# Optimization experiments

Measured on AMD Instinct MI355X. Metric: run time of the kernel, lower is better.

## Reference

```python
import jax, jax.numpy as jnp
import numpy as np

NUM_HEADS = 6

def setup_inputs() -> dict:
    key = jax.random.key(0)
    k1, k2, k3, k4 = jax.random.split(key, 4)
    B, N, C = 8, 2048, 384
    x = jax.random.normal(k1, (B, N, C), dtype=jnp.float32)
    qkv_w = jax.random.normal(k2, (3 * C, C), dtype=jnp.float32) * (C ** -0.5)
    proj_w = jax.random.normal(k3, (C, C), dtype=jnp.float32) * (C ** -0.5)
    proj_b = jax.random.normal(k4, (C,), dtype=jnp.float32) * 0.01
    temperature = jnp.ones((NUM_HEADS, 1, 1), dtype=jnp.float32)
    return {"x": x, "qkv_w": qkv_w, "proj_w": proj_w, "proj_b": proj_b,
            "temperature": temperature}


def reference(x, qkv_w, proj_w, proj_b, temperature):
    B, N, C = x.shape
    H = NUM_HEADS
    Dh = C // H
    # qkv projection (no bias), split into q, k, v per head
    qkv = (x @ qkv_w.T).reshape(B, N, 3, H, Dh)
    qkv = jnp.transpose(qkv, (2, 0, 3, 1, 4))  # [3, B, H, N, Dh]
    q, k, v = qkv[0], qkv[1], qkv[2]
    # scores scaled by sqrt(C) (full dim, as in source), then learnable temperature
    attn = jnp.einsum('bhnd,bhmd->bhnm', q, k) / (C ** 0.5)
    attn = attn / temperature  # temperature: [H,1,1] broadcasts over B and N,N
    # diagonal (self-token) mask -> -inf before softmax
    diag = jnp.eye(N, dtype=bool)
    attn = jnp.where(diag, -jnp.inf, attn)
    attn = jax.nn.softmax(attn, axis=-1)
    # attend and merge heads
    out = jnp.einsum('bhnm,bhmd->bhnd', attn, v)
    out = jnp.transpose(out, (0, 2, 1, 3)).reshape(B, N, C)
    # output projection
    return out @ proj_w.T + proj_b
```

## Files before the change

### kernel.cpp

```cpp
#include <hip/hip_runtime.h>


using f32x4 = __attribute__((ext_vector_type(4))) float;
using s16x8 = __attribute__((ext_vector_type(8))) short;
using u16x4 = __attribute__((ext_vector_type(4))) unsigned short;
using u32x2 = __attribute__((ext_vector_type(2))) unsigned int;
using u32x4 = __attribute__((ext_vector_type(4))) unsigned int;
typedef unsigned short u16;
typedef unsigned int u32;

#define MFMA16(a, b, c) __builtin_amdgcn_mfma_f32_16x16x32_bf16(a, b, c, 0, 0, 0)
#define LOG2E 1.4426950408889634f
#define SQRTC 19.595917942265423f

__device__ __forceinline__ u16 f2bf(float f) {
  u32 u = __float_as_uint(f);
  u += 0x7fffu + ((u >> 16) & 1u);
  return (u16)(u >> 16);
}

__device__ __forceinline__ u32 cvtpk(float lo, float hi) {
  u32 r;
  asm("v_cvt_pk_bf16_f32 %0, %1, %2" : "=v"(r) : "v"(lo), "v"(hi));
  return r;
}

__device__ __forceinline__ float fexp2(float x) {
  float r;
  asm("v_exp_f32 %0, %1" : "=v"(r) : "v"(x));
  return r;
}

__device__ __forceinline__ void gld16(const void* g, void* l) {
  __builtin_amdgcn_global_load_lds((const __attribute__((address_space(1))) void*)g,
                                   (__attribute__((address_space(3))) void*)l, 16, 0, 0);
}

__global__ __launch_bounds__(256) void k_cvt2(const float* __restrict__ A,
                                              u16* __restrict__ Oa,
                                              const float* __restrict__ B,
                                              u16* __restrict__ Ob) {
  const int bid = blockIdx.x;
  const float* in;
  u16* out;
  size_t i;
  if (bid < 432) { in = A; out = Oa; i = (size_t)bid * 256 + threadIdx.x; }
  else           { in = B; out = Ob; i = (size_t)(bid - 432) * 256 + threadIdx.x; }
  f32x4 v = *(const f32x4*)(in + i * 4);
  u16x4 o;
  o[0] = f2bf(v[0]); o[1] = f2bf(v[1]); o[2] = f2bf(v[2]); o[3] = f2bf(v[3]);
  *(u16x4*)(out + i * 4) = o;
}

__global__ __launch_bounds__(256) void k_qkv(const float* __restrict__ X,
                                             const u16* __restrict__ W,
                                             const float* __restrict__ temp,
                                             u16* __restrict__ Qt,
                                             u16* __restrict__ Kb,
                                             u16* __restrict__ Vt) {
  __shared__ u16 As[2][128 * 32];
  __shared__ u16 Bs[2][128 * 32];
  const int tid = threadIdx.x, w = tid >> 6, l = tid & 63, lr = l & 15, lg = l >> 4;
  const int id = blockIdx.y * 9 + blockIdx.x;
  const int swz = (id & 7) * 144 + (id >> 3);
  const int tn = (swz % 9) * 128, tm = (swz / 9) * 128;
  const int wr = w >> 1, wc = w & 1;
  const int r0 = tid >> 2, c8 = (tid & 3) * 8;
  const int ar = tid >> 1, ac = (tid & 1) * 16;

  f32x4 acc[4][4] = {};
  f32x4 a4[4];

  auto issueA = [&](int kt) {
    const float* xp = X + (size_t)(tm + ar) * 384 + kt * 32 + ac;
    a4[0] = *(const f32x4*)(xp);
    a4[1] = *(const f32x4*)(xp + 4);
    a4[2] = *(const f32x4*)(xp + 8);
    a4[3] = *(const f32x4*)(xp + 12);
  };
  auto commitA = [&](int buf) {
    u32x4 h0, h1;
    h0[0] = cvtpk(a4[0][0], a4[0][1]); h0[1] = cvtpk(a4[0][2], a4[0][3]);
    h0[2] = cvtpk(a4[1][0], a4[1][1]); h0[3] = cvtpk(a4[1][2], a4[1][3]);
    h1[0] = cvtpk(a4[2][0], a4[2][1]); h1[1] = cvtpk(a4[2][2], a4[2][3]);
    h1[2] = cvtpk(a4[3][0], a4[3][1]); h1[3] = cvtpk(a4[3][2], a4[3][3]);
    *(u32x4*)&As[buf][ar * 32 + ac] = h0;
    *(u32x4*)&As[buf][ar * 32 + ac + 8] = h1;
  };
  auto stageB = [&](int buf, int kt) {
    const int k0 = kt * 32;
    char* db = (char*)(&Bs[buf][0]) + (w << 10);
    gld16(W + (size_t)(tn + r0) * 384 + k0 + c8, db);
    gld16(W + (size_t)(tn + 64 + r0) * 384 + k0 + c8, db + 4096);
  };

  issueA(0); stageB(0, 0); commitA(0);
  for (int kt = 0; kt < 12; ++kt) {
    __syncthreads();
    if (kt < 11) { issueA(kt + 1); stageB((kt + 1) & 1, kt + 1); }
    const int buf = kt & 1;
    s16x8 af[4], bfr[4];
    for (int mi = 0; mi < 4; mi++)
      af[mi] = *(const s16x8*)&As[buf][(wr * 64 + mi * 16 + lr) * 32 + lg * 8];
    for (int ni = 0; ni < 4; ni++)
      bfr[ni] = *(const s16x8*)&Bs[buf][(wc * 64 + ni * 16 + lr) * 32 + lg * 8];
    for (int mi = 0; mi < 4; mi++)
      for (int ni = 0; ni < 4; ni++)
        acc[mi][ni] = MFMA16(af[mi], bfr[ni], acc[mi][ni]);
    if (kt < 11) commitA((kt + 1) & 1);
  }

  const int which = (tn + wc * 64) / 384;
  const int bidx = (tm >> 11);
  for (int mi = 0; mi < 4; mi++)
    for (int ni = 0; ni < 4; ni++) {
      const int n = tn + wc * 64 + ni * 16 + lr;
      const int c = n - which * 384;
      const int h = c >> 6, d = c & 63;
      const size_t bh = (size_t)(bidx * 6 + h);
      if (which == 1) {
        for (int j = 0; j < 4; j++) {
          const int pos = (tm + wr * 64 + mi * 16 + lg * 4 + j) & 2047;
          Kb[(bh * 2048 + pos) * 64 + d] = f2bf(acc[mi][ni][j]);
        }
      } else {
        const float mult = (which == 0) ? (LOG2E / (SQRTC * temp[h])) : 1.0f;
        const int pos0 = (tm + wr * 64 + mi * 16 + lg * 4) & 2047;
        u16x4 vv;
        vv[0] = f2bf(acc[mi][ni][0] * mult); vv[1] = f2bf(acc[mi][ni][1] * mult);
        vv[2] = f2bf(acc[mi][ni][2] * mult); vv[3] = f2bf(acc[mi][ni][3] * mult);
        u16* dst = (which == 0) ? Qt : Vt;
        *(u16x4*)&dst[(bh * 64 + d) * 2048 + pos0] = vv;
      }
    }
}

#define LDSOFF(row, c16) (((row) * 128 + (c16) * 16) ^ (((row) & 7) << 4))

__global__ __launch_bounds__(256, 3) void k_attn(const u16* __restrict__ Qt,
                                                 const u16* __restrict__ Kb,
                                                 const u16* __restrict__ Vt,
                                                 u16* __restrict__ AO) {
  __shared__ u16 Ks[2][64 * 64];
  __shared__ u16 Vs[2][64 * 64];
  const int tid = threadIdx.x, w = tid >> 6, l = tid & 63, lr = l & 15, lg = l >> 4;
  const int orig = blockIdx.x;
  const int rm = (orig & 7) * 96 + (orig >> 3);
  const int qt = rm & 15, bh = rm >> 4;
  const int h = bh % 6, b = bh / 6;
  const size_t base = (size_t)bh << 17;
  const int q0 = qt * 128 + w * 32;
  const int maskKt = q0 >> 6;
  const int qo = q0 & 63;

  s16x8 qf[2][2];
  for (int mi = 0; mi < 2; mi++)
    for (int ks = 0; ks < 2; ks++) {
      const u16* qp = Qt + base + (size_t)(ks * 32 + lg * 8) * 2048 + q0 + mi * 16 + lr;
      s16x8 q;
      for (int e = 0; e < 8; ++e) q[e] = (short)qp[(size_t)e * 2048];
      qf[mi][ks] = q;
    }

  s16x8 ones;
  for (int e = 0; e < 8; ++e) ones[e] = (short)0x3F80;

  f32x4 o0[4] = {}, o1[4] = {};
  f32x4 os0 = {}, os1 = {};

  const int r0 = tid >> 3, c0 = tid & 7;
  const int c8 = c0 * 8;
  const int wo0 = LDSOFF(r0, c0), wo1 = LDSOFF(r0 + 32, c0);

  s16x8 ka0, ka1, va0, va1;
  auto issue = [&](int kt) {
    const u16* kp = Kb + base + (size_t)(kt * 64 + r0) * 64 + c8;
    ka0 = *(const s16x8*)kp;
    ka1 = *(const s16x8*)(kp + 32 * 64);
    const u16* vp = Vt + base + (size_t)r0 * 2048 + kt * 64 + c8;
    va0 = *(const s16x8*)vp;
    va1 = *(const s16x8*)(vp + 32 * 2048);
  };
  auto commit = [&](int buf) {
    char* kd = (char*)&Ks[buf][0];
    char* vd = (char*)&Vs[buf][0];
    *(s16x8*)(kd + wo0) = ka0; *(s16x8*)(kd + wo1) = ka1;
    *(s16x8*)(vd + wo0) = va0; *(s16x8*)(vd + wo1) = va1;
  };

  issue(0); commit(0);
  __syncthreads();

  const int lrs = (lr & 7) << 4;
  const int x0 = (lg * 16) ^ lrs;
  const int x1 = (64 + lg * 16) ^ lrs;
  const int vo0 = (lg * 8) ^ lrs;
  const int vo1 = (32 + lg * 8) ^ lrs;
  const int vo2 = (64 + lg * 8) ^ lrs;
  const int vo3 = (96 + lg * 8) ^ lrs;

  for (int kt = 0; kt < 32; ++kt) {
    const int cur = kt & 1;
    if (kt < 31) issue(kt + 1);

    f32x4 st0[4] = {}, st1[4] = {};
    const char* kbp = (const char*)&Ks[cur][0];
    __builtin_amdgcn_s_setprio(1);
    for (int ni = 0; ni < 4; ++ni) {
      const int rb = (ni * 16 + lr) * 128;
      const s16x8 kf0 = *(const s16x8*)(kbp + (rb + x0));
      const s16x8 kf1 = *(const s16x8*)(kbp + (rb + x1));
      st0[ni] = MFMA16(kf0, qf[0][0], st0[ni]);
      st0[ni] = MFMA16(kf1, qf[0][1], st0[ni]);
      st1[ni] = MFMA16(kf0, qf[1][0], st1[ni]);
      st1[ni] = MFMA16(kf1, qf[1][1], st1[ni]);
    }
    __builtin_amdgcn_s_setprio(0);

    if (kt == maskKt) {
      for (int ni = 0; ni < 4; ++ni)
        for (int j = 0; j < 4; ++j) {
          const int kvl = ni * 16 + lg * 4 + j;
          if (kvl == qo + lr)      st0[ni][j] = -1e30f;
          if (kvl == qo + 16 + lr) st1[ni][j] = -1e30f;
        }
    }

    const char* vbp = (const char*)&Vs[cur][0];
    s16x8 vfr[2][4];
    for (int dj = 0; dj < 4; ++dj) {
      const int rb = (dj * 16 + lr) * 128;
      u32x2 a = *(const u32x2*)(vbp + rb + vo0);
      u32x2 bq = *(const u32x2*)(vbp + rb + vo1);
      u32x2 c = *(const u32x2*)(vbp + rb + vo2);
      u32x2 d = *(const u32x2*)(vbp + rb + vo3);
      u32x4 t0; t0[0] = a[0]; t0[1] = a[1]; t0[2] = bq[0]; t0[3] = bq[1];
      u32x4 t1; t1[0] = c[0]; t1[1] = c[1]; t1[2] = d[0]; t1[3] = d[1];
      vfr[0][dj] = __builtin_bit_cast(s16x8, t0);
      vfr[1][dj] = __builtin_bit_cast(s16x8, t1);
    }

    {
      u32 pk[8];
      for (int ni = 0; ni < 4; ++ni) {
        pk[ni * 2]     = cvtpk(fexp2(st0[ni][0]), fexp2(st0[ni][1]));
        pk[ni * 2 + 1] = cvtpk(fexp2(st0[ni][2]), fexp2(st0[ni][3]));
      }
      u32x4 a0; a0[0] = pk[0]; a0[1] = pk[1]; a0[2] = pk[2]; a0[3] = pk[3];
      u32x4 a1; a1[0] = pk[4]; a1[1] = pk[5]; a1[2] = pk[6]; a1[3] = pk[7];
      const s16x8 pa0 = __builtin_bit_cast(s16x8, a0);
      const s16x8 pa1 = __builtin_bit_cast(s16x8, a1);
      __builtin_amdgcn_s_setprio(1);
      for (int dj = 0; dj < 4; ++dj) o0[dj] = MFMA16(pa0, vfr[0][dj], o0[dj]);
      os0 = MFMA16(pa0, ones, os0);
      for (int dj = 0; dj < 4; ++dj) o0[dj] = MFMA16(pa1, vfr[1][dj], o0[dj]);
      os0 = MFMA16(pa1, ones, os0);
      __builtin_amdgcn_s_setprio(0);
    }
    {
      u32 pk[8];
      for (int ni = 0; ni < 4; ++ni) {
        pk[ni * 2]     = cvtpk(fexp2(st1[ni][0]), fexp2(st1[ni][1]));
        pk[ni * 2 + 1] = cvtpk(fexp2(st1[ni][2]), fexp2(st1[ni][3]));
      }
      u32x4 a0; a0[0] = pk[0]; a0[1] = pk[1]; a0[2] = pk[2]; a0[3] = pk[3];
      u32x4 a1; a1[0] = pk[4]; a1[1] = pk[5]; a1[2] = pk[6]; a1[3] = pk[7];
      const s16x8 pa0 = __builtin_bit_cast(s16x8, a0);
      const s16x8 pa1 = __builtin_bit_cast(s16x8, a1);
      __builtin_amdgcn_s_setprio(1);
      for (int dj = 0; dj < 4; ++dj) o1[dj] = MFMA16(pa0, vfr[0][dj], o1[dj]);
      os1 = MFMA16(pa0, ones, os1);
      for (int dj = 0; dj < 4; ++dj) o1[dj] = MFMA16(pa1, vfr[1][dj], o1[dj]);
      os1 = MFMA16(pa1, ones, os1);
      __builtin_amdgcn_s_setprio(0);
    }

    if (kt < 31) commit(cur ^ 1);
    __syncthreads();
  }

  f32x4 rv0, rv1;
  for (int j = 0; j < 4; ++j) { rv0[j] = 1.0f / os0[j]; rv1[j] = 1.0f / os1[j]; }
  const size_t aobase = (size_t)b * 2048 * 384 + (size_t)h * 64;
  for (int j = 0; j < 4; ++j) {
    const int pos0 = q0 + lg * 4 + j;
    const int pos1 = pos0 + 16;
    for (int dj = 0; dj < 4; ++dj) {
      AO[aobase + (size_t)pos0 * 384 + dj * 16 + lr] = f2bf(o0[dj][j] * rv0[j]);
      AO[aobase + (size_t)pos1 * 384 + dj * 16 + lr] = f2bf(o1[dj][j] * rv1[j]);
    }
  }
}

__global__ __launch_bounds__(256) void k_proj(const u16* __restrict__ A,
                                              const u16* __restrict__ W,
                                              const float* __restrict__ bias,
                                              float* __restrict__ out) {
  __shared__ u16 As[2][128 * 32];
  __shared__ u16 Bs[2][64 * 32];
  const int tid = threadIdx.x, w = tid >> 6, l = tid & 63, lr = l & 15, lg = l >> 4;
  const int id = blockIdx.y * 6 + blockIdx.x;
  const int swz = (id & 7) * 96 + (id >> 3);
  const int tn = (swz % 6) * 64, tm = (swz / 6) * 128;
  const int r0 = tid >> 2, c8 = (tid & 3) * 8;

  f32x4 acc[2][4] = {};

  auto stage = [&](int buf, int kt) {
    const int k0 = kt * 32;
    char* da = (char*)(&As[buf][0]) + (w << 10);
    char* db = (char*)(&Bs[buf][0]) + (w << 10);
    gld16(A + (size_t)(tm + r0) * 384 + k0 + c8, da);
    gld16(A + (size_t)(tm + 64 + r0) * 384 + k0 + c8, da + 4096);
    gld16(W + (size_t)(tn + r0) * 384 + k0 + c8, db);
  };

  stage(0, 0);
  for (int kt = 0; kt < 12; ++kt) {
    __syncthreads();
    if (kt < 11) stage((kt + 1) & 1, kt + 1);
    const int buf = kt & 1;
    s16x8 af[2], bfr[4];
    for (int mi = 0; mi < 2; mi++)
      af[mi] = *(const s16x8*)&As[buf][(w * 32 + mi * 16 + lr) * 32 + lg * 8];
    for (int ni = 0; ni < 4; ni++)
      bfr[ni] = *(const s16x8*)&Bs[buf][(ni * 16 + lr) * 32 + lg * 8];
    for (int mi = 0; mi < 2; mi++)
      for (int ni = 0; ni < 4; ni++)
        acc[mi][ni] = MFMA16(af[mi], bfr[ni], acc[mi][ni]);
  }

  for (int mi = 0; mi < 2; mi++)
    for (int ni = 0; ni < 4; ni++) {
      const int n = tn + ni * 16 + lr;
      const float bn = bias[n];
      for (int j = 0; j < 4; j++) {
        const int m = tm + w * 32 + mi * 16 + lg * 4 + j;
        out[(size_t)m * 384 + n] = acc[mi][ni][j] + bn;
      }
    }
}

extern "C" void kernel_launch(void* const* d_in, const int* in_sizes, int n_in,
                              void* d_out, int out_size, void* d_ws, size_t ws_size,
                              hipStream_t stream) {
  const float* x      = (const float*)d_in[0];
  const float* qkv_w  = (const float*)d_in[1];
  const float* proj_w = (const float*)d_in[2];
  const float* proj_b = (const float*)d_in[3];
  const float* temp   = (const float*)d_in[4];
  float* out = (float*)d_out;

  u16* wqkvb  = (u16*)d_ws;
  u16* wprojb = wqkvb + 442368;
  u16* Qt     = wprojb + 147456;
  u16* Kb     = Qt + 6291456;
  u16* Vtb    = Kb + 6291456;
  u16* AOb    = Vtb + 6291456;

  k_cvt2<<<576, 256, 0, stream>>>(qkv_w, wqkvb, proj_w, wprojb);
  k_qkv<<<dim3(9, 128), 256, 0, stream>>>(x, wqkvb, temp, Qt, Kb, Vtb);
  k_attn<<<768, 256, 0, stream>>>(Qt, Kb, Vtb, AOb);
  k_proj<<<dim3(6, 128), 256, 0, stream>>>(AOb, wprojb, proj_b, out);
}
```

Before: 121.0 us.

## Double KV tile to 128 keys per iteration with split K/V prefetch

```diff
diff --git a/kernel.cpp b/kernel.cpp
--- a/kernel.cpp
+++ b/kernel.cpp
@@ -135,14 +135,15 @@
     }
 }
 
-#define LDSOFF(row, c16) (((row) * 128 + (c16) * 16) ^ (((row) & 7) << 4))
-
-__global__ __launch_bounds__(256, 3) void k_attn(const u16* __restrict__ Qt,
+#define KLDSOFF(row, c16) (((row) * 128 + (c16) * 16) ^ (((row) & 7) << 4))
+#define VLDSOFF(dd, c16) (((dd) * 256 + (c16) * 16) ^ (((dd) & 15) << 4))
+
+__global__ __launch_bounds__(256, 2) void k_attn(const u16* __restrict__ Qt,
                                                  const u16* __restrict__ Kb,
                                                  const u16* __restrict__ Vt,
                                                  u16* __restrict__ AO) {
-  __shared__ u16 Ks[2][64 * 64];
-  __shared__ u16 Vs[2][64 * 64];
+  __shared__ u16 Ks[2][128 * 64];
+  __shared__ u16 Vs[2][64 * 128];
   const int tid = threadIdx.x, w = tid >> 6, l = tid & 63, lr = l & 15, lg = l >> 4;
   const int orig = blockIdx.x;
   const int rm = (orig & 7) * 96 + (orig >> 3);
@@ -150,8 +151,8 @@
   const int h = bh % 6, b = bh / 6;
   const size_t base = (size_t)bh << 17;
   const int q0 = qt * 128 + w * 32;
-  const int maskKt = q0 >> 6;
-  const int qo = q0 & 63;
+  const int maskKt = q0 >> 7;
+  const int qo = q0 & 127;
 
   s16x8 qf[2][2];
   for (int mi = 0; mi < 2; mi++)
@@ -168,57 +169,66 @@
   f32x4 o0[4] = {}, o1[4] = {};
   f32x4 os0 = {}, os1 = {};
 
-  const int r0 = tid >> 3, c0 = tid & 7;
-  const int c8 = c0 * 8;
-  const int wo0 = LDSOFF(r0, c0), wo1 = LDSOFF(r0 + 32, c0);
-
-  s16x8 ka0, ka1, va0, va1;
-  auto issue = [&](int kt) {
-    const u16* kp = Kb + base + (size_t)(kt * 64 + r0) * 64 + c8;
-    ka0 = *(const s16x8*)kp;
-    ka1 = *(const s16x8*)(kp + 32 * 64);
-    const u16* vp = Vt + base + (size_t)r0 * 2048 + kt * 64 + c8;
-    va0 = *(const s16x8*)vp;
-    va1 = *(const s16x8*)(vp + 32 * 2048);
-  };
-  auto commit = [&](int buf) {
+  const int kr = tid >> 3, kc = tid & 7;
+  const int vr = tid >> 4, vc = tid & 15;
+
+  s16x8 ka[4], va[4];
+  auto issueK = [&](int kt) {
+    const u16* kp = Kb + base + (size_t)(kt * 128 + kr) * 64 + kc * 8;
+    ka[0] = *(const s16x8*)kp;
+    ka[1] = *(const s16x8*)(kp + 32 * 64);
+    ka[2] = *(const s16x8*)(kp + 64 * 64);
+    ka[3] = *(const s16x8*)(kp + 96 * 64);
+  };
+  auto issueV = [&](int kt) {
+    const u16* vp = Vt + base + (size_t)vr * 2048 + kt * 128 + vc * 8;
+    va[0] = *(const s16x8*)vp;
+    va[1] = *(const s16x8*)(vp + 16 * 2048);
+    va[2] = *(const s16x8*)(vp + 32 * 2048);
+    va[3] = *(const s16x8*)(vp + 48 * 2048);
+  };
+  auto commitKV = [&](int buf) {
     char* kd = (char*)&Ks[buf][0];
+    *(s16x8*)(kd + KLDSOFF(kr, kc))      = ka[0];
+    *(s16x8*)(kd + KLDSOFF(kr + 32, kc)) = ka[1];
+    *(s16x8*)(kd + KLDSOFF(kr + 64, kc)) = ka[2];
+    *(s16x8*)(kd + KLDSOFF(kr + 96, kc)) = ka[3];
     char* vd = (char*)&Vs[buf][0];
-    *(s16x8*)(kd + wo0) = ka0; *(s16x8*)(kd + wo1) = ka1;
-    *(s16x8*)(vd + wo0) = va0; *(s16x8*)(vd + wo1) = va1;
-  };
-
-  issue(0); commit(0);
+    *(s16x8*)(vd + VLDSOFF(vr, vc))      = va[0];
+    *(s16x8*)(vd + VLDSOFF(vr + 16, vc)) = va[1];
+    *(s16x8*)(vd + VLDSOFF(vr + 32, vc)) = va[2];
+    *(s16x8*)(vd + VLDSOFF(vr + 48, vc)) = va[3];
+  };
+
+  issueK(0); issueV(0); commitKV(0);
   __syncthreads();
 
-  const int lrs = (lr & 7) << 4;
-  const int x0 = (lg * 16) ^ lrs;
-  const int x1 = (64 + lg * 16) ^ lrs;
-  const int vo0 = (lg * 8) ^ lrs;
-  const int vo1 = (32 + lg * 8) ^ lrs;
-  const int vo2 = (64 + lg * 8) ^ lrs;
-  const int vo3 = (96 + lg * 8) ^ lrs;
-
-  for (int kt = 0; kt < 32; ++kt) {
+  const int lrs7 = (lr & 7) << 4;
+  const int kx0 = (lg * 16) ^ lrs7;
+  const int kx1 = (64 + lg * 16) ^ lrs7;
+  const int vswz = lr << 4;
+
+  for (int kt = 0; kt < 16; ++kt) {
     const int cur = kt & 1;
-    if (kt < 31) issue(kt + 1);
-
-    f32x4 st0[4] = {}, st1[4] = {};
+    if (kt < 15) issueK(kt + 1);
+
+    f32x4 st0[8], st1[8];
     const char* kbp = (const char*)&Ks[cur][0];
     __builtin_amdgcn_s_setprio(1);
-    for (int ni = 0; ni < 4; ++ni) {
+    for (int ni = 0; ni < 8; ++ni) {
       const int rb = (ni * 16 + lr) * 128;
-      const s16x8 kf0 = *(const s16x8*)(kbp + (rb + x0));
-      const s16x8 kf1 = *(const s16x8*)(kbp + (rb + x1));
-      st0[ni] = MFMA16(kf0, qf[0][0], st0[ni]);
+      const s16x8 kf0 = *(const s16x8*)(kbp + (rb + kx0));
+      const s16x8 kf1 = *(const s16x8*)(kbp + (rb + kx1));
+      f32x4 z = {};
+      st0[ni] = MFMA16(kf0, qf[0][0], z);
       st0[ni] = MFMA16(kf1, qf[0][1], st0[ni]);
-      st1[ni] = MFMA16(kf0, qf[1][0], st1[ni]);
+      st1[ni] = MFMA16(kf0, qf[1][0], z);
       st1[ni] = MFMA16(kf1, qf[1][1], st1[ni]);
     }
     __builtin_amdgcn_s_setprio(0);
 
     if (kt == maskKt) {
-      for (int ni = 0; ni < 4; ++ni)
+      for (int ni = 0; ni < 8; ++ni)
         for (int j = 0; j < 4; ++j) {
           const int kvl = ni * 16 + lg * 4 + j;
           if (kvl == qo + lr)      st0[ni][j] = -1e30f;
@@ -226,56 +236,42 @@
         }
     }
 
+    u32 pk0[16], pk1[16];
+    for (int ni = 0; ni < 8; ++ni) {
+      pk0[ni * 2]     = cvtpk(fexp2(st0[ni][0]), fexp2(st0[ni][1]));
+      pk0[ni * 2 + 1] = cvtpk(fexp2(st0[ni][2]), fexp2(st0[ni][3]));
+    }
+    if (kt < 15) issueV(kt + 1);
+    for (int ni = 0; ni < 8; ++ni) {
+      pk1[ni * 2]     = cvtpk(fexp2(st1[ni][0]), fexp2(st1[ni][1]));
+      pk1[ni * 2 + 1] = cvtpk(fexp2(st1[ni][2]), fexp2(st1[ni][3]));
+    }
+
     const char* vbp = (const char*)&Vs[cur][0];
-    s16x8 vfr[2][4];
-    for (int dj = 0; dj < 4; ++dj) {
-      const int rb = (dj * 16 + lr) * 128;
-      u32x2 a = *(const u32x2*)(vbp + rb + vo0);
-      u32x2 bq = *(const u32x2*)(vbp + rb + vo1);
-      u32x2 c = *(const u32x2*)(vbp + rb + vo2);
-      u32x2 d = *(const u32x2*)(vbp + rb + vo3);
-      u32x4 t0; t0[0] = a[0]; t0[1] = a[1]; t0[2] = bq[0]; t0[3] = bq[1];
-      u32x4 t1; t1[0] = c[0]; t1[1] = c[1]; t1[2] = d[0]; t1[3] = d[1];
-      vfr[0][dj] = __builtin_bit_cast(s16x8, t0);
-      vfr[1][dj] = __builtin_bit_cast(s16x8, t1);
-    }
-
-    {
-      u32 pk[8];
-      for (int ni = 0; ni < 4; ++ni) {
-        pk[ni * 2]     = cvtpk(fexp2(st0[ni][0]), fexp2(st0[ni][1]));
-        pk[ni * 2 + 1] = cvtpk(fexp2(st0[ni][2]), fexp2(st0[ni][3]));
+    for (int c = 0; c < 4; ++c) {
+      s16x8 vfr[4];
+      for (int dj = 0; dj < 4; ++dj) {
+        const int rb = (dj * 16 + lr) * 256;
+        u32x2 aa = *(const u32x2*)(vbp + rb + ((c * 64 + lg * 8) ^ vswz));
+        u32x2 bb = *(const u32x2*)(vbp + rb + ((c * 64 + 32 + lg * 8) ^ vswz));
+        u32x4 t; t[0] = aa[0]; t[1] = aa[1]; t[2] = bb[0]; t[3] = bb[1];
+        vfr[dj] = __builtin_bit_cast(s16x8, t);
       }
-      u32x4 a0; a0[0] = pk[0]; a0[1] = pk[1]; a0[2] = pk[2]; a0[3] = pk[3];
-      u32x4 a1; a1[0] = pk[4]; a1[1] = pk[5]; a1[2] = pk[6]; a1[3] = pk[7];
-      const s16x8 pa0 = __builtin_bit_cast(s16x8, a0);
-      const s16x8 pa1 = __builtin_bit_cast(s16x8, a1);
+      u32x4 p0v; p0v[0] = pk0[c * 4]; p0v[1] = pk0[c * 4 + 1];
+      p0v[2] = pk0[c * 4 + 2]; p0v[3] = pk0[c * 4 + 3];
+      u32x4 p1v; p1v[0] = pk1[c * 4]; p1v[1] = pk1[c * 4 + 1];
+      p1v[2] = pk1[c * 4 + 2]; p1v[3] = pk1[c * 4 + 3];
+      const s16x8 pa0 = __builtin_bit_cast(s16x8, p0v);
+      const s16x8 pa1 = __builtin_bit_cast(s16x8, p1v);
       __builtin_amdgcn_s_setprio(1);
-      for (int dj = 0; dj < 4; ++dj) o0[dj] = MFMA16(pa0, vfr[0][dj], o0[dj]);
+      for (int dj = 0; dj < 4; ++dj) o0[dj] = MFMA16(pa0, vfr[dj], o0[dj]);
       os0 = MFMA16(pa0, ones, os0);
-      for (int dj = 0; dj < 4; ++dj) o0[dj] = MFMA16(pa1, vfr[1][dj], o0[dj]);
-      os0 = MFMA16(pa1, ones, os0);
-      __builtin_amdgcn_s_setprio(0);
-    }
-    {
-      u32 pk[8];
-      for (int ni = 0; ni < 4; ++ni) {
-        pk[ni * 2]     = cvtpk(fexp2(st1[ni][0]), fexp2(st1[ni][1]));
-        pk[ni * 2 + 1] = cvtpk(fexp2(st1[ni][2]), fexp2(st1[ni][3]));
-      }
-      u32x4 a0; a0[0] = pk[0]; a0[1] = pk[1]; a0[2] = pk[2]; a0[3] = pk[3];
-      u32x4 a1; a1[0] = pk[4]; a1[1] = pk[5]; a1[2] = pk[6]; a1[3] = pk[7];
-      const s16x8 pa0 = __builtin_bit_cast(s16x8, a0);
-      const s16x8 pa1 = __builtin_bit_cast(s16x8, a1);
-      __builtin_amdgcn_s_setprio(1);
-      for (int dj = 0; dj < 4; ++dj) o1[dj] = MFMA16(pa0, vfr[0][dj], o1[dj]);
-      os1 = MFMA16(pa0, ones, os1);
-      for (int dj = 0; dj < 4; ++dj) o1[dj] = MFMA16(pa1, vfr[1][dj], o1[dj]);
+      for (int dj = 0; dj < 4; ++dj) o1[dj] = MFMA16(pa1, vfr[dj], o1[dj]);
       os1 = MFMA16(pa1, ones, os1);
       __builtin_amdgcn_s_setprio(0);
     }
 
-    if (kt < 31) commit(cur ^ 1);
+    if (kt < 15) commitKV(cur ^ 1);
     __syncthreads();
   }
 
```

After: 127.8 us. 1.06x slower.
